# Kernel optimization log

Hardware: AMD Instinct MI355X
Metric: run time of the kernel (lower is better)

The kernel has to match this reference:

```python
import jax, jax.numpy as jnp
import numpy as np
import math

B, SQ, SK, DQ, DK = 16, 2048, 2048, 1024, 1024

def setup_inputs() -> dict:
    key = jax.random.key(0)
    ks = jax.random.split(key, 6)
    return {
        "bert_feature": jax.random.normal(ks[0], (B, SQ, DQ), dtype=jnp.float32),
        "knowledge_feature": jax.random.normal(ks[1], (B, SK, DK), dtype=jnp.float32),
        "w1_w": jax.random.normal(ks[2], (DK, DQ), dtype=jnp.float32) * 0.02,
        "w1_b": jax.random.normal(ks[3], (DK,), dtype=jnp.float32) * 0.02,
        "w2_w": jax.random.normal(ks[4], (DQ, DQ + DK), dtype=jnp.float32) * 0.02,
        "w2_b": jax.random.normal(ks[5], (DQ,), dtype=jnp.float32) * 0.02,
    }

def reference(bert_feature, knowledge_feature, w1_w, w1_b, w2_w, w2_b):
    d_k = knowledge_feature.shape[-1]
    # w1 projection: [B, Sq, d_q] -> [B, Sq, d_k]
    bf = jnp.einsum('bqd,kd->bqk', bert_feature, w1_w) + w1_b
    # scaled dot-product attention with knowledge as K and V
    scores = jnp.einsum('bqd,bkd->bqk', bf, knowledge_feature) / math.sqrt(d_k)
    attn = jax.nn.softmax(scores, axis=-1)
    output = jnp.einsum('bqk,bkd->bqd', attn, knowledge_feature)
    # concat + fusion linear: [B, Sq, d_q + d_k] -> [B, Sq, d_q]
    fused = jnp.concatenate([bert_feature, output], axis=-1)
    return jnp.einsum('bqf,of->bqo', fused, w2_w) + w2_b
```

## Files before the change

### kernel.cpp

```cpp
#include <hip/hip_runtime.h>

typedef __attribute__((ext_vector_type(8))) short s16x8;
typedef __attribute__((ext_vector_type(8))) unsigned short u16x8;
typedef __attribute__((ext_vector_type(4))) unsigned short u16x4;
typedef __attribute__((ext_vector_type(4))) float f32x4;

__device__ inline float bf2f(unsigned short h) {
  union { unsigned int u; float f; } x; x.u = ((unsigned int)h) << 16; return x.f;
}
__device__ inline unsigned short f2bf(float f) {
  union { float f; unsigned int u; } x; x.f = f;
  unsigned int u = x.u;
  return (unsigned short)((u + 0x7fffu + ((u >> 16) & 1u)) >> 16);
}

__global__ __launch_bounds__(256) void cvt_bf16(const float* __restrict__ in,
                                                unsigned short* __restrict__ out,
                                                long long n, int shift, int ldo) {
  long long i = (long long)blockIdx.x * 256 + threadIdx.x;
  long long stride = (long long)gridDim.x * 256;
  long long nchunks = n >> 3;
  for (; i < nchunks; i += stride) {
    long long e = i << 3;
    long long r = e >> shift;
    int c = (int)(e & ((1LL << shift) - 1));
    const float4* p = (const float4*)(in + e);
    float4 f0 = p[0], f1 = p[1];
    u16x8 u;
    u[0] = f2bf(f0.x); u[1] = f2bf(f0.y); u[2] = f2bf(f0.z); u[3] = f2bf(f0.w);
    u[4] = f2bf(f1.x); u[5] = f2bf(f1.y); u[6] = f2bf(f1.z); u[7] = f2bf(f1.w);
    *(u16x8*)&out[r * (long long)ldo + c] = u;
  }
}

__global__ __launch_bounds__(256) void cvt_transpose(const float* __restrict__ in,
                                                     unsigned short* __restrict__ out_n,
                                                     unsigned short* __restrict__ out_t,
                                                     int rows, int cols) {
  __shared__ unsigned short tile[64][72];
  long long zoff = (long long)blockIdx.z * rows * cols;
  const float* src = in + zoff;
  unsigned short* dstn = out_n + zoff;
  unsigned short* dstt = out_t + zoff;
  int k0 = blockIdx.x * 64, d0 = blockIdx.y * 64;
  int t = threadIdx.x;
  int rr = t >> 4;
  int cc = (t & 15) * 4;
#pragma unroll
  for (int i = 0; i < 4; ++i) {
    int k = rr + i * 16;
    float4 v = *(const float4*)&src[(long long)(k0 + k) * cols + d0 + cc];
    u16x4 u;
    u[0] = f2bf(v.x); u[1] = f2bf(v.y); u[2] = f2bf(v.z); u[3] = f2bf(v.w);
    *(u16x4*)&dstn[(long long)(k0 + k) * cols + d0 + cc] = u;
    *(u16x4*)&tile[k][cc] = u;
  }
  __syncthreads();
#pragma unroll
  for (int i = 0; i < 4; ++i) {
    int d = rr + i * 16;
    u16x4 v;
#pragma unroll
    for (int j = 0; j < 4; ++j) v[j] = tile[cc + j][d];
    *(u16x4*)&dstt[(long long)(d0 + d) * rows + k0 + cc] = v;
  }
}

__global__ __launch_bounds__(256) void rowsum_inv(const float* __restrict__ part,
                                                  float* __restrict__ rinv, int nrows) {
  int i = blockIdx.x * 256 + threadIdx.x;
  if (i < nrows) {
    const float* p = part + (long long)i * 8;
    float s = 0.f;
#pragma unroll
    for (int k = 0; k < 8; ++k) s += p[k];
    rinv[i] = 1.0f / s;
  }
}

template <bool OUT_BF16, bool HAS_BIAS, bool EXP_SM, bool ROWSCALE>
__global__ __launch_bounds__(512, 1) void gemm256(
    const unsigned short* __restrict__ A, const unsigned short* __restrict__ Bt,
    void* __restrict__ C, const float* __restrict__ bias,
    int K, int lda, int ldb, int ldc,
    long long sA, long long sB, long long sC, float scale,
    int gx, int gy, float* __restrict__ part, const float* __restrict__ rinv) {
  __shared__ char lds[131072];
  const int t = threadIdx.x;
  const int l = t & 63, w = t >> 6;
  const int wm = w >> 2, wn = w & 3;

  const int nwg = gridDim.x;
  const int id = blockIdx.x;
  const int sid = (id & 7) * (nwg >> 3) + (id >> 3);
  const int bx = sid % gx;
  const int rem = sid / gx;
  const int by = rem % gy;
  const int bz = rem / gy;

  A += (long long)bz * sA;
  Bt += (long long)bz * sB;
  const long long m0 = (long long)by * 256;
  const long long n0 = (long long)bx * 256;

  const int trow = t >> 2;
  const int kl8 = ((t & 3) ^ ((t >> 3) & 3)) * 8;
  const unsigned short* gA = A + (m0 + trow) * lda + kl8;
  const unsigned short* gB = Bt + (n0 + trow) * ldb + kl8;
  const int Lt = t * 16;

  const int lo = (l & 15) * 64 + ((((l >> 4) ^ (((l & 15) >> 1) & 3))) << 4);

  f32x4 acc[8][4] = {};
  const int nt = K >> 6;

#define STAGE_A(KT, KSL)                                                             \
  {                                                                                  \
    char* d_ = lds + (((KT) & 1) * 65536) + ((KSL) * 16384);                         \
    const unsigned short* g_ = gA + (long long)(KT) * 64 + (KSL) * 32;               \
    __builtin_amdgcn_global_load_lds(                                                \
        (const __attribute__((address_space(1))) void*)g_,                           \
        (__attribute__((address_space(3))) void*)(d_ + Lt), 16, 0, 0);               \
    __builtin_amdgcn_global_load_lds(                                                \
        (const __attribute__((address_space(1))) void*)(g_ + 128 * lda),             \
        (__attribute__((address_space(3))) void*)(d_ + 8192 + Lt), 16, 0, 0);        \
  }
#define STAGE_B(KT, KSL)                                                             \
  {                                                                                  \
    char* d_ = lds + (((KT) & 1) * 65536) + 32768 + ((KSL) * 16384);                 \
    const unsigned short* g_ = gB + (long long)(KT) * 64 + (KSL) * 32;               \
    __builtin_amdgcn_global_load_lds(                                                \
        (const __attribute__((address_space(1))) void*)g_,                           \
        (__attribute__((address_space(3))) void*)(d_ + Lt), 16, 0, 0);               \
    __builtin_amdgcn_global_load_lds(                                                \
        (const __attribute__((address_space(1))) void*)(g_ + 128 * ldb),             \
        (__attribute__((address_space(3))) void*)(d_ + 8192 + Lt), 16, 0, 0);        \
  }

  STAGE_A(0, 0); STAGE_A(0, 1); STAGE_B(0, 0); STAGE_B(0, 1);
  STAGE_B(1, 0); STAGE_A(1, 0); STAGE_B(1, 1);
  asm volatile("s_waitcnt vmcnt(6)" ::: "memory");
  __builtin_amdgcn_s_barrier();

  s16x8 af[4], bf[4];

#define READ_A(MH, KSL, CB)                                                          \
  _Pragma("unroll")                                                                  \
  for (int m_ = 0; m_ < 4; ++m_)                                                     \
    af[m_] = *(const s16x8*)((CB) + (KSL) * 16384 + wm * 8192 + ((MH) * 4 + m_) * 1024 + lo);
#define READ_B(KSL, CB)                                                              \
  _Pragma("unroll")                                                                  \
  for (int n_ = 0; n_ < 4; ++n_)                                                     \
    bf[n_] = *(const s16x8*)((CB) + 32768 + (KSL) * 16384 + wn * 4096 + n_ * 1024 + lo);
#define MFMA_Q(MH)                                                                   \
  __builtin_amdgcn_s_setprio(1);                                                     \
  _Pragma("unroll")                                                                  \
  for (int m_ = 0; m_ < 4; ++m_)                                                     \
    _Pragma("unroll")                                                                \
    for (int n_ = 0; n_ < 4; ++n_)                                                   \
      acc[(MH) * 4 + m_][n_] =                                                       \
          __builtin_amdgcn_mfma_f32_16x16x32_bf16(af[m_], bf[n_], acc[(MH) * 4 + m_][n_], 0, 0, 0); \
  __builtin_amdgcn_s_setprio(0);
#define BAR __builtin_amdgcn_s_barrier()
#define LGKM0 asm volatile("s_waitcnt lgkmcnt(0)" ::: "memory")

  for (int kt = 0; kt < nt; ++kt) {
    const char* cb = lds + (kt & 1) * 65536;
    const bool p1 = (kt + 1 < nt), p2 = (kt + 2 < nt);
    READ_B(0, cb); READ_A(0, 0, cb);
    if (p1) STAGE_A(kt + 1, 1);
    BAR; LGKM0; MFMA_Q(0); BAR;
    READ_A(1, 0, cb);
    if (p2) STAGE_B(kt + 2, 0);
    BAR; LGKM0; MFMA_Q(1); BAR;
    READ_B(1, cb); READ_A(0, 1, cb);
    if (p2) STAGE_A(kt + 2, 0);
    BAR; LGKM0; MFMA_Q(0); BAR;
    READ_A(1, 1, cb);
    if (p2) STAGE_B(kt + 2, 1);
    BAR; LGKM0; MFMA_Q(1);
    if (p2)      asm volatile("s_waitcnt vmcnt(6)" ::: "memory");
    else         asm volatile("s_waitcnt vmcnt(0)" ::: "memory");
    BAR;
  }
#undef STAGE_A
#undef STAGE_B
#undef READ_A
#undef READ_B
#undef MFMA_Q
#undef BAR
#undef LGKM0

  const int cl = l & 15, rg = (l >> 4) * 4;

  if (EXP_SM) {
    float* pl = (float*)lds;
#pragma unroll
    for (int m = 0; m < 8; ++m) {
#pragma unroll
      for (int j = 0; j < 4; ++j) {
        float s = 0.f;
#pragma unroll
        for (int n = 0; n < 4; ++n) {
          float e = __expf(acc[m][n][j]);
          acc[m][n][j] = e;
          s += e;
        }
        s += __shfl_xor(s, 1); s += __shfl_xor(s, 2);
        s += __shfl_xor(s, 4); s += __shfl_xor(s, 8);
        if (cl == 0) pl[wn * 256 + wm * 128 + m * 16 + rg + j] = s;
      }
    }
    __syncthreads();
    if (t < 256) {
      float s = pl[t] + pl[256 + t] + pl[512 + t] + pl[768 + t];
      part[((long long)bz * 2048 + m0 + t) * 8 + bx] = s;
    }
  }

#pragma unroll
  for (int m = 0; m < 8; ++m) {
    long long row = m0 + wm * 128 + m * 16 + rg;
    float rv[4];
    if (ROWSCALE) {
#pragma unroll
      for (int j = 0; j < 4; ++j) rv[j] = rinv[(long long)bz * 2048 + row + j];
    }
#pragma unroll
    for (int n = 0; n < 4; ++n) {
      long long col = n0 + wn * 64 + n * 16 + cl;
      float bb = HAS_BIAS ? bias[col] : 0.0f;
#pragma unroll
      for (int j = 0; j < 4; ++j) {
        float v = EXP_SM ? acc[m][n][j] : (acc[m][n][j] + bb) * scale;
        if (ROWSCALE) v *= rv[j];
        if (OUT_BF16)
          ((unsigned short*)C)[bz * sC + (row + j) * ldc + col] = f2bf(v);
        else
          ((float*)C)[bz * sC + (row + j) * ldc + col] = v;
      }
    }
  }
}

extern "C" void kernel_launch(void* const* d_in, const int* in_sizes, int n_in,
                              void* d_out, int out_size, void* d_ws, size_t ws_size,
                              hipStream_t stream) {
  const float* bert = (const float*)d_in[0];
  const float* know = (const float*)d_in[1];
  const float* w1w  = (const float*)d_in[2];
  const float* w1b  = (const float*)d_in[3];
  const float* w2w  = (const float*)d_in[4];
  const float* w2b  = (const float*)d_in[5];

  char* ws = (char*)d_ws;
  unsigned short* fused  = (unsigned short*)(ws);
  unsigned short* bfq    = (unsigned short*)(ws + 134217728LL);
  unsigned short* know16 = (unsigned short*)(ws + 201326592LL);
  unsigned short* knowT  = (unsigned short*)(ws + 268435456LL);
  unsigned short* w1_16  = (unsigned short*)(ws + 335544320LL);
  unsigned short* w2_16  = (unsigned short*)(ws + 337641472LL);
  float*          part   = (float*)(ws + 341835776LL);
  float*          rinv   = (float*)(ws + 342884352LL);
  unsigned short* P      = (unsigned short*)d_out;

  cvt_bf16<<<2048, 256, 0, stream>>>(bert, fused, 33554432LL, 10, 2048);
  cvt_bf16<<<512, 256, 0, stream>>>(w1w, w1_16, 1048576LL, 10, 1024);
  cvt_bf16<<<512, 256, 0, stream>>>(w2w, w2_16, 2097152LL, 11, 2048);
  cvt_transpose<<<dim3(32, 16, 16), 256, 0, stream>>>(know, know16, knowT, 2048, 1024);

  gemm256<true, true, false, false><<<4 * 128, 512, 0, stream>>>(
      fused, w1_16, bfq, w1b, 1024, 2048, 1024, 1024, 0, 0, 0, 0.03125f, 4, 128,
      nullptr, nullptr);

  gemm256<true, false, true, false><<<8 * 8 * 16, 512, 0, stream>>>(
      bfq, know16, P, nullptr, 1024, 1024, 1024, 2048,
      2048LL * 1024, 2048LL * 1024, 2048LL * 2048, 1.0f, 8, 8,
      part, nullptr);

  rowsum_inv<<<128, 256, 0, stream>>>(part, rinv, 32768);

  gemm256<true, false, false, true><<<4 * 8 * 16, 512, 0, stream>>>(
      P, knowT, fused + 1024, nullptr, 2048, 2048, 2048, 2048,
      2048LL * 2048, 1024LL * 2048, 2048LL * 2048, 1.0f, 4, 8,
      nullptr, rinv);

  gemm256<false, true, false, false><<<4 * 128, 512, 0, stream>>>(
      fused, w2_16, d_out, w2b, 2048, 2048, 2048, 1024, 0, 0, 0, 1.0f, 4, 128,
      nullptr, nullptr);
}
```

Measured before the change: 625.1 us.

## Use triple-buffered 128x256 GEMM kernel for final fusion projection

```diff
diff --git a/kernel.cpp b/kernel.cpp
--- a/kernel.cpp
+++ b/kernel.cpp
@@ -243,6 +243,114 @@
   }
 }
 
+template <bool OUT_BF16, bool HAS_BIAS>
+__global__ __launch_bounds__(256, 2) void gemm_r3(
+    const unsigned short* __restrict__ A, const unsigned short* __restrict__ Bt,
+    void* __restrict__ C, const float* __restrict__ bias,
+    int K, int lda, int ldb, int ldc,
+    long long sA, long long sB, long long sC, float scale,
+    int gx, int gy) {
+  __shared__ char lds[73728];
+  const int t = threadIdx.x;
+  const int l = t & 63, w = t >> 6;
+  const int wm = w >> 1, wn = w & 1;
+
+  const int nwg = gridDim.x;
+  const int id = blockIdx.x;
+  const int sid = (id & 7) * (nwg >> 3) + (id >> 3);
+  const int bx = sid % gx;
+  const int rem = sid / gx;
+  const int by = rem % gy;
+  const int bz = rem / gy;
+
+  A += (long long)bz * sA;
+  Bt += (long long)bz * sB;
+  const long long m0 = (long long)by * 128;
+  const long long n0 = (long long)bx * 256;
+
+  const int srow = t >> 2;
+  const int sk = (((t & 3) * 16) ^ (((t >> 3) & 3) << 4)) >> 1;
+  const unsigned short* gA = A + (m0 + srow) * lda + sk;
+  const unsigned short* gB = Bt + (n0 + srow) * ldb + sk;
+  const int Lt = t * 16;
+
+  const int lo = (l & 15) * 64 + ((((l >> 4) ^ (((l & 15) >> 1) & 3))) << 4);
+
+  f32x4 acc[4][8] = {};
+  const int nt = K >> 5;
+
+#define STAGE(J)                                                                     \
+  {                                                                                  \
+    char* s_ = lds + (((J) % 3) * 24576);                                            \
+    long long ko_ = (long long)(J) * 32;                                             \
+    __builtin_amdgcn_global_load_lds(                                                \
+        (const __attribute__((address_space(1))) void*)(gA + ko_),                   \
+        (__attribute__((address_space(3))) void*)(s_ + Lt), 16, 0, 0);               \
+    __builtin_amdgcn_global_load_lds(                                                \
+        (const __attribute__((address_space(1))) void*)(gA + 64 * lda + ko_),        \
+        (__attribute__((address_space(3))) void*)(s_ + 4096 + Lt), 16, 0, 0);        \
+    __builtin_amdgcn_global_load_lds(                                                \
+        (const __attribute__((address_space(1))) void*)(gB + ko_),                   \
+        (__attribute__((address_space(3))) void*)(s_ + 8192 + Lt), 16, 0, 0);        \
+    __builtin_amdgcn_global_load_lds(                                                \
+        (const __attribute__((address_space(1))) void*)(gB + 64 * ldb + ko_),        \
+        (__attribute__((address_space(3))) void*)(s_ + 12288 + Lt), 16, 0, 0);       \
+    __builtin_amdgcn_global_load_lds(                                                \
+        (const __attribute__((address_space(1))) void*)(gB + 128 * ldb + ko_),       \
+        (__attribute__((address_space(3))) void*)(s_ + 16384 + Lt), 16, 0, 0);       \
+    __builtin_amdgcn_global_load_lds(                                                \
+        (const __attribute__((address_space(1))) void*)(gB + 192 * ldb + ko_),       \
+        (__attribute__((address_space(3))) void*)(s_ + 20480 + Lt), 16, 0, 0);       \
+  }
+
+  STAGE(0); STAGE(1);
+  asm volatile("s_waitcnt vmcnt(6)" ::: "memory");
+  __builtin_amdgcn_s_barrier();
+
+  for (int j = 0; j < nt; ++j) {
+    if (j + 2 < nt) STAGE(j + 2);
+    const char* s_ = lds + ((j % 3) * 24576);
+    const char* sa = s_ + wm * 4096;
+    const char* sb = s_ + 8192 + wn * 8192;
+    s16x8 af[4], bf[8];
+#pragma unroll
+    for (int m = 0; m < 4; ++m) af[m] = *(const s16x8*)(sa + m * 1024 + lo);
+#pragma unroll
+    for (int n = 0; n < 8; ++n) bf[n] = *(const s16x8*)(sb + n * 1024 + lo);
+    asm volatile("s_waitcnt lgkmcnt(0)" ::: "memory");
+    __builtin_amdgcn_s_setprio(1);
+#pragma unroll
+    for (int m = 0; m < 4; ++m)
+#pragma unroll
+      for (int n = 0; n < 8; ++n)
+        acc[m][n] = __builtin_amdgcn_mfma_f32_16x16x32_bf16(af[m], bf[n], acc[m][n], 0, 0, 0);
+    __builtin_amdgcn_s_setprio(0);
+    if (j + 2 < nt) asm volatile("s_waitcnt vmcnt(6)" ::: "memory");
+    else            asm volatile("s_waitcnt vmcnt(0)" ::: "memory");
+    __builtin_amdgcn_s_barrier();
+  }
+#undef STAGE
+
+  const int cl = l & 15, rg = (l >> 4) * 4;
+#pragma unroll
+  for (int m = 0; m < 4; ++m) {
+#pragma unroll
+    for (int n = 0; n < 8; ++n) {
+      long long col = n0 + wn * 128 + n * 16 + cl;
+      long long row = m0 + wm * 64 + m * 16 + rg;
+      float bb = HAS_BIAS ? bias[col] : 0.0f;
+#pragma unroll
+      for (int j = 0; j < 4; ++j) {
+        float v = (acc[m][n][j] + bb) * scale;
+        if (OUT_BF16)
+          ((unsigned short*)C)[bz * sC + (row + j) * ldc + col] = f2bf(v);
+        else
+          ((float*)C)[bz * sC + (row + j) * ldc + col] = v;
+      }
+    }
+  }
+}
+
 extern "C" void kernel_launch(void* const* d_in, const int* in_sizes, int n_in,
                               void* d_out, int out_size, void* d_ws, size_t ws_size,
                               hipStream_t stream) {
@@ -285,7 +393,6 @@
       2048LL * 2048, 1024LL * 2048, 2048LL * 2048, 1.0f, 4, 8,
       nullptr, rinv);
 
-  gemm256<false, true, false, false><<<4 * 128, 512, 0, stream>>>(
-      fused, w2_16, d_out, w2b, 2048, 2048, 2048, 1024, 0, 0, 0, 1.0f, 4, 128,
-      nullptr, nullptr);
-}
+  gemm_r3<false, true><<<4 * 256, 256, 0, stream>>>(
+      fused, w2_16, d_out, w2b, 2048, 2048, 2048, 1024, 0, 0, 0, 1.0f, 4, 256);
+}
```

After: 633.3 us. Within noise of the previous version (+1.3%).

## Make GEMM kernels persistent and prefetch next tile during epilogue

Applied to the files above, without the earlier changes.

```diff
diff --git a/kernel.cpp b/kernel.cpp
--- a/kernel.cpp
+++ b/kernel.cpp
@@ -69,13 +69,7 @@
 __global__ __launch_bounds__(256) void rowsum_inv(const float* __restrict__ part,
                                                   float* __restrict__ rinv, int nrows) {
   int i = blockIdx.x * 256 + threadIdx.x;
-  if (i < nrows) {
-    const float* p = part + (long long)i * 8;
-    float s = 0.f;
-#pragma unroll
-    for (int k = 0; k < 8; ++k) s += p[k];
-    rinv[i] = 1.0f / s;
-  }
+  if (i < nrows) rinv[i] = 1.0f / part[i];
 }
 
 template <bool OUT_BF16, bool HAS_BIAS, bool EXP_SM, bool ROWSCALE>
@@ -84,7 +78,8 @@
     void* __restrict__ C, const float* __restrict__ bias,
     int K, int lda, int ldb, int ldc,
     long long sA, long long sB, long long sC, float scale,
-    int gx, int gy, float* __restrict__ part, const float* __restrict__ rinv) {
+    int gx, int gy, int ntiles, float* __restrict__ part,
+    const float* __restrict__ rinv) {
   __shared__ char lds[131072];
   const int t = threadIdx.x;
   const int l = t & 63, w = t >> 6;
@@ -93,57 +88,40 @@
   const int nwg = gridDim.x;
   const int id = blockIdx.x;
   const int sid = (id & 7) * (nwg >> 3) + (id >> 3);
-  const int bx = sid % gx;
-  const int rem = sid / gx;
-  const int by = rem % gy;
-  const int bz = rem / gy;
-
-  A += (long long)bz * sA;
-  Bt += (long long)bz * sB;
-  const long long m0 = (long long)by * 256;
-  const long long n0 = (long long)bx * 256;
 
   const int trow = t >> 2;
   const int kl8 = ((t & 3) ^ ((t >> 3) & 3)) * 8;
-  const unsigned short* gA = A + (m0 + trow) * lda + kl8;
-  const unsigned short* gB = Bt + (n0 + trow) * ldb + kl8;
   const int Lt = t * 16;
-
   const int lo = (l & 15) * 64 + ((((l >> 4) ^ (((l & 15) >> 1) & 3))) << 4);
-
-  f32x4 acc[8][4] = {};
   const int nt = K >> 6;
-
-#define STAGE_A(KT, KSL)                                                             \
+  const int cl = l & 15, rg = (l >> 4) * 4;
+  const f32x4 zero4 = {0.f, 0.f, 0.f, 0.f};
+
+  f32x4 acc[8][4];
+
+#define GLOAD(SRC, DST)                                                              \
+  __builtin_amdgcn_global_load_lds(                                                  \
+      (const __attribute__((address_space(1))) void*)(SRC),                          \
+      (__attribute__((address_space(3))) void*)(DST), 16, 0, 0)
+#define STAGE_A(GP, KT, KSL)                                                         \
   {                                                                                  \
     char* d_ = lds + (((KT) & 1) * 65536) + ((KSL) * 16384);                         \
-    const unsigned short* g_ = gA + (long long)(KT) * 64 + (KSL) * 32;               \
-    __builtin_amdgcn_global_load_lds(                                                \
-        (const __attribute__((address_space(1))) void*)g_,                           \
-        (__attribute__((address_space(3))) void*)(d_ + Lt), 16, 0, 0);               \
-    __builtin_amdgcn_global_load_lds(                                                \
-        (const __attribute__((address_space(1))) void*)(g_ + 128 * lda),             \
-        (__attribute__((address_space(3))) void*)(d_ + 8192 + Lt), 16, 0, 0);        \
-  }
-#define STAGE_B(KT, KSL)                                                             \
+    const unsigned short* g_ = (GP) + (long long)(KT) * 64 + (KSL) * 32;             \
+    GLOAD(g_, d_ + Lt);                                                              \
+    GLOAD(g_ + 128 * lda, d_ + 8192 + Lt);                                           \
+  }
+#define STAGE_B(GP, KT, KSL)                                                         \
   {                                                                                  \
     char* d_ = lds + (((KT) & 1) * 65536) + 32768 + ((KSL) * 16384);                 \
-    const unsigned short* g_ = gB + (long long)(KT) * 64 + (KSL) * 32;               \
-    __builtin_amdgcn_global_load_lds(                                                \
-        (const __attribute__((address_space(1))) void*)g_,                           \
-        (__attribute__((address_space(3))) void*)(d_ + Lt), 16, 0, 0);               \
-    __builtin_amdgcn_global_load_lds(                                                \
-        (const __attribute__((address_space(1))) void*)(g_ + 128 * ldb),             \
-        (__attribute__((address_space(3))) void*)(d_ + 8192 + Lt), 16, 0, 0);        \
-  }
-
-  STAGE_A(0, 0); STAGE_A(0, 1); STAGE_B(0, 0); STAGE_B(0, 1);
-  STAGE_B(1, 0); STAGE_A(1, 0); STAGE_B(1, 1);
-  asm volatile("s_waitcnt vmcnt(6)" ::: "memory");
-  __builtin_amdgcn_s_barrier();
-
-  s16x8 af[4], bf[4];
-
+    const unsigned short* g_ = (GP) + (long long)(KT) * 64 + (KSL) * 32;             \
+    GLOAD(g_, d_ + Lt);                                                              \
+    GLOAD(g_ + 128 * ldb, d_ + 8192 + Lt);                                           \
+  }
+#define PROLOG(GA, GB)                                                               \
+  {                                                                                  \
+    STAGE_A(GA, 0, 0); STAGE_A(GA, 0, 1); STAGE_B(GB, 0, 0); STAGE_B(GB, 0, 1);      \
+    STAGE_B(GB, 1, 0); STAGE_A(GA, 1, 0); STAGE_B(GB, 1, 1);                         \
+  }
 #define READ_A(MH, KSL, CB)                                                          \
   _Pragma("unroll")                                                                  \
   for (int m_ = 0; m_ < 4; ++m_)                                                     \
@@ -164,83 +142,123 @@
 #define BAR __builtin_amdgcn_s_barrier()
 #define LGKM0 asm volatile("s_waitcnt lgkmcnt(0)" ::: "memory")
 
-  for (int kt = 0; kt < nt; ++kt) {
-    const char* cb = lds + (kt & 1) * 65536;
-    const bool p1 = (kt + 1 < nt), p2 = (kt + 2 < nt);
-    READ_B(0, cb); READ_A(0, 0, cb);
-    if (p1) STAGE_A(kt + 1, 1);
-    BAR; LGKM0; MFMA_Q(0); BAR;
-    READ_A(1, 0, cb);
-    if (p2) STAGE_B(kt + 2, 0);
-    BAR; LGKM0; MFMA_Q(1); BAR;
-    READ_B(1, cb); READ_A(0, 1, cb);
-    if (p2) STAGE_A(kt + 2, 0);
-    BAR; LGKM0; MFMA_Q(0); BAR;
-    READ_A(1, 1, cb);
-    if (p2) STAGE_B(kt + 2, 1);
-    BAR; LGKM0; MFMA_Q(1);
-    if (p2)      asm volatile("s_waitcnt vmcnt(6)" ::: "memory");
-    else         asm volatile("s_waitcnt vmcnt(0)" ::: "memory");
+  long long m0, n0;
+  int bz;
+  const unsigned short *gA, *gB;
+  {
+    const int tile = sid;
+    const int bx = tile % gx;
+    const int rem = tile / gx;
+    const int by = rem % gy;
+    bz = rem / gy;
+    m0 = (long long)by * 256;
+    n0 = (long long)bx * 256;
+    gA = A + bz * sA + (m0 + trow) * lda + kl8;
+    gB = Bt + bz * sB + (n0 + trow) * ldb + kl8;
+  }
+  PROLOG(gA, gB);
+
+  for (int tile = sid; tile < ntiles; tile += nwg) {
+    asm volatile("s_waitcnt vmcnt(6)" ::: "memory");
     BAR;
-  }
+#pragma unroll
+    for (int m = 0; m < 8; ++m)
+#pragma unroll
+      for (int n = 0; n < 4; ++n) acc[m][n] = zero4;
+
+    s16x8 af[4], bf[4];
+    for (int kt = 0; kt < nt; ++kt) {
+      const char* cb = lds + (kt & 1) * 65536;
+      const bool p1 = (kt + 1 < nt), p2 = (kt + 2 < nt);
+      READ_B(0, cb); READ_A(0, 0, cb);
+      if (p1) STAGE_A(gA, kt + 1, 1);
+      BAR; LGKM0; MFMA_Q(0); BAR;
+      READ_A(1, 0, cb);
+      if (p2) STAGE_B(gB, kt + 2, 0);
+      BAR; LGKM0; MFMA_Q(1); BAR;
+      READ_B(1, cb); READ_A(0, 1, cb);
+      if (p2) STAGE_A(gA, kt + 2, 0);
+      BAR; LGKM0; MFMA_Q(0); BAR;
+      READ_A(1, 1, cb);
+      if (p2) STAGE_B(gB, kt + 2, 1);
+      BAR; LGKM0; MFMA_Q(1);
+      if (p2)      asm volatile("s_waitcnt vmcnt(6)" ::: "memory");
+      else         asm volatile("s_waitcnt vmcnt(0)" ::: "memory");
+      BAR;
+    }
+    const bool more = (tile + nwg) < ntiles;
+    long long m0n = 0, n0n = 0;
+    int bzn = 0;
+    const unsigned short *gAn = gA, *gBn = gB;
+    if (more) {
+      const int tl = tile + nwg;
+      const int bx = tl % gx;
+      const int rem = tl / gx;
+      const int by = rem % gy;
+      bzn = rem / gy;
+      m0n = (long long)by * 256;
+      n0n = (long long)bx * 256;
+      gAn = A + bzn * sA + (m0n + trow) * lda + kl8;
+      gBn = Bt + bzn * sB + (n0n + trow) * ldb + kl8;
+      PROLOG(gAn, gBn);
+    }
+
+    if (EXP_SM) {
+#pragma unroll
+      for (int m = 0; m < 8; ++m) {
+#pragma unroll
+        for (int j = 0; j < 4; ++j) {
+          float s = 0.f;
+#pragma unroll
+          for (int n = 0; n < 4; ++n) {
+            float e = __expf(acc[m][n][j]);
+            acc[m][n][j] = e;
+            s += e;
+          }
+          s += __shfl_xor(s, 1); s += __shfl_xor(s, 2);
+          s += __shfl_xor(s, 4); s += __shfl_xor(s, 8);
+          if (cl == 0)
+            atomicAdd(&part[(long long)bz * 2048 + m0 + wm * 128 + m * 16 + rg + j], s);
+        }
+      }
+    }
+#pragma unroll
+    for (int m = 0; m < 8; ++m) {
+      long long row = m0 + wm * 128 + m * 16 + rg;
+      float rv[4];
+      if (ROWSCALE) {
+#pragma unroll
+        for (int j = 0; j < 4; ++j) rv[j] = rinv[(long long)bz * 2048 + row + j];
+      }
+#pragma unroll
+      for (int n = 0; n < 4; ++n) {
+        long long col = n0 + wn * 64 + n * 16 + cl;
+        float bb = HAS_BIAS ? bias[col] : 0.0f;
+#pragma unroll
+        for (int j = 0; j < 4; ++j) {
+          float v = EXP_SM ? acc[m][n][j] : (acc[m][n][j] + bb) * scale;
+          if (ROWSCALE) v *= rv[j];
+          if (OUT_BF16)
+            ((unsigned short*)C)[bz * sC + (row + j) * ldc + col] = f2bf(v);
+          else
+            ((float*)C)[bz * sC + (row + j) * ldc + col] = v;
+        }
+      }
+    }
+
+    asm volatile("s_waitcnt vmcnt(0)" ::: "memory");
+    BAR;
+    if (more) { m0 = m0n; n0 = n0n; bz = bzn; gA = gAn; gB = gBn; }
+  }
+#undef GLOAD
 #undef STAGE_A
 #undef STAGE_B
+#undef PROLOG
 #undef READ_A
 #undef READ_B
 #undef MFMA_Q
 #undef BAR
 #undef LGKM0
-
-  const int cl = l & 15, rg = (l >> 4) * 4;
-
-  if (EXP_SM) {
-    float* pl = (float*)lds;
-#pragma unroll
-    for (int m = 0; m < 8; ++m) {
-#pragma unroll
-      for (int j = 0; j < 4; ++j) {
-        float s = 0.f;
-#pragma unroll
-        for (int n = 0; n < 4; ++n) {
-          float e = __expf(acc[m][n][j]);
-          acc[m][n][j] = e;
-          s += e;
-        }
-        s += __shfl_xor(s, 1); s += __shfl_xor(s, 2);
-        s += __shfl_xor(s, 4); s += __shfl_xor(s, 8);
-        if (cl == 0) pl[wn * 256 + wm * 128 + m * 16 + rg + j] = s;
-      }
-    }
-    __syncthreads();
-    if (t < 256) {
-      float s = pl[t] + pl[256 + t] + pl[512 + t] + pl[768 + t];
-      part[((long long)bz * 2048 + m0 + t) * 8 + bx] = s;
-    }
-  }
-
-#pragma unroll
-  for (int m = 0; m < 8; ++m) {
-    long long row = m0 + wm * 128 + m * 16 + rg;
-    float rv[4];
-    if (ROWSCALE) {
-#pragma unroll
-      for (int j = 0; j < 4; ++j) rv[j] = rinv[(long long)bz * 2048 + row + j];
-    }
-#pragma unroll
-    for (int n = 0; n < 4; ++n) {
-      long long col = n0 + wn * 64 + n * 16 + cl;
-      float bb = HAS_BIAS ? bias[col] : 0.0f;
-#pragma unroll
-      for (int j = 0; j < 4; ++j) {
-        float v = EXP_SM ? acc[m][n][j] : (acc[m][n][j] + bb) * scale;
-        if (ROWSCALE) v *= rv[j];
-        if (OUT_BF16)
-          ((unsigned short*)C)[bz * sC + (row + j) * ldc + col] = f2bf(v);
-        else
-          ((float*)C)[bz * sC + (row + j) * ldc + col] = v;
-      }
-    }
-  }
 }
 
 extern "C" void kernel_launch(void* const* d_in, const int* in_sizes, int n_in,
@@ -264,28 +282,29 @@
   float*          rinv   = (float*)(ws + 342884352LL);
   unsigned short* P      = (unsigned short*)d_out;
 
+  hipMemsetAsync(part, 0, 32768 * sizeof(float), stream);
   cvt_bf16<<<2048, 256, 0, stream>>>(bert, fused, 33554432LL, 10, 2048);
   cvt_bf16<<<512, 256, 0, stream>>>(w1w, w1_16, 1048576LL, 10, 1024);
   cvt_bf16<<<512, 256, 0, stream>>>(w2w, w2_16, 2097152LL, 11, 2048);
   cvt_transpose<<<dim3(32, 16, 16), 256, 0, stream>>>(know, know16, knowT, 2048, 1024);
 
-  gemm256<true, true, false, false><<<4 * 128, 512, 0, stream>>>(
-      fused, w1_16, bfq, w1b, 1024, 2048, 1024, 1024, 0, 0, 0, 0.03125f, 4, 128,
-      nullptr, nullptr);
-
-  gemm256<true, false, true, false><<<8 * 8 * 16, 512, 0, stream>>>(
+  gemm256<true, true, false, false><<<256, 512, 0, stream>>>(
+      fused, w1_16, bfq, w1b, 1024, 2048, 1024, 1024, 0, 0, 0, 0.03125f,
+      4, 128, 512, nullptr, nullptr);
+
+  gemm256<true, false, true, false><<<256, 512, 0, stream>>>(
       bfq, know16, P, nullptr, 1024, 1024, 1024, 2048,
-      2048LL * 1024, 2048LL * 1024, 2048LL * 2048, 1.0f, 8, 8,
-      part, nullptr);
+      2048LL * 1024, 2048LL * 1024, 2048LL * 2048, 1.0f,
+      8, 8, 1024, part, nullptr);
 
   rowsum_inv<<<128, 256, 0, stream>>>(part, rinv, 32768);
 
-  gemm256<true, false, false, true><<<4 * 8 * 16, 512, 0, stream>>>(
+  gemm256<true, false, false, true><<<256, 512, 0, stream>>>(
       P, knowT, fused + 1024, nullptr, 2048, 2048, 2048, 2048,
-      2048LL * 2048, 1024LL * 2048, 2048LL * 2048, 1.0f, 4, 8,
-      nullptr, rinv);
-
-  gemm256<false, true, false, false><<<4 * 128, 512, 0, stream>>>(
-      fused, w2_16, d_out, w2b, 2048, 2048, 2048, 1024, 0, 0, 0, 1.0f, 4, 128,
-      nullptr, nullptr);
-}
+      2048LL * 2048, 1024LL * 2048, 2048LL * 2048, 1.0f,
+      4, 8, 512, nullptr, rinv);
+
+  gemm256<false, true, false, false><<<256, 512, 0, stream>>>(
+      fused, w2_16, d_out, w2b, 2048, 2048, 2048, 1024, 0, 0, 0, 1.0f,
+      4, 128, 512, nullptr, nullptr);
+}
```

Result: no change. 623.2 us (-0.3%).
